# Optimization experiments

Hardware: AMD Instinct MI355X
Metric: run time of the kernel (lower is better)

## Reference

```python
import jax, jax.numpy as jnp
import numpy as np

B, D, H = 1024, 64, 128


def setup_inputs() -> dict:
    key = jax.random.key(0)
    ks = jax.random.split(key, 12)
    s1 = 1.0 / np.sqrt(4 * D)
    sh = 1.0 / np.sqrt(H)
    sd = 1.0 / np.sqrt(D)
    return {
        "x": jax.random.normal(ks[0], (B, D), dtype=jnp.float32),
        # edge_fn: Linear(4D,H) -> ReLU -> Linear(H,H)
        "W1": jax.random.uniform(ks[1], (4 * D, H), minval=-s1, maxval=s1, dtype=jnp.float32),
        "b1": jax.random.uniform(ks[2], (H,), minval=-s1, maxval=s1, dtype=jnp.float32),
        "W2": jax.random.uniform(ks[3], (H, H), minval=-sh, maxval=sh, dtype=jnp.float32),
        "b2": jax.random.uniform(ks[4], (H,), minval=-sh, maxval=sh, dtype=jnp.float32),
        # tau_proj: Linear(D,1) -> Softplus
        "Wt": jax.random.uniform(ks[5], (D, 1), minval=-sd, maxval=sd, dtype=jnp.float32),
        "bt": jax.random.uniform(ks[6], (1,), minval=-sd, maxval=sd, dtype=jnp.float32),
        # agg: Linear(H,H) -> ReLU
        "Wa": jax.random.uniform(ks[7], (H, H), minval=-sh, maxval=sh, dtype=jnp.float32),
        "ba": jax.random.uniform(ks[8], (H,), minval=-sh, maxval=sh, dtype=jnp.float32),
        # res_proj: Linear(D,H)
        "Wr": jax.random.uniform(ks[9], (D, H), minval=-sd, maxval=sd, dtype=jnp.float32),
        "br": jax.random.uniform(ks[10], (H,), minval=-sd, maxval=sd, dtype=jnp.float32),
        # LayerNorm(H)
        "gamma": jnp.ones((H,), dtype=jnp.float32),
        "beta": jnp.zeros((H,), dtype=jnp.float32),
    }


def reference(x, W1, b1, W2, b2, Wt, bt, Wa, ba, Wr, br, gamma, beta):
    d = x.shape[1]
    # Decompose first linear over concat([x_i, x_j, delta, |delta|]) into 4 sub-matmuls;
    # only the |delta| term needs the pairwise [B,B,D] tensor.
    Wi, Wj, Wd, Wab = W1[:d], W1[d:2 * d], W1[2 * d:3 * d], W1[3 * d:]
    ti = x @ Wi            # [B,H] (i-dependent)
    tj = x @ Wj            # [B,H] (j-dependent)
    td = x @ Wd            # [B,H] (delta = x_i - x_j contribution)
    delta = x[:, None, :] - x[None, :, :]             # [B,B,D]
    ta = jnp.einsum('ijd,dh->ijh', jnp.abs(delta), Wab)  # [B,B,H]
    pre = ti[:, None, :] + tj[None, :, :] + td[:, None, :] - td[None, :, :] + ta + b1
    d_proj = jax.nn.relu(pre) @ W2 + b2               # [B,B,H]
    tau = jnp.maximum(jax.nn.softplus(x @ Wt + bt), 0.01) + 1.0  # [B,1]
    h_mean = d_proj.mean(axis=1) / tau                # mean over j
    h = jax.nn.relu(h_mean @ Wa + ba)
    y = h + (x @ Wr + br)
    mu = y.mean(axis=-1, keepdims=True)
    var = ((y - mu) ** 2).mean(axis=-1, keepdims=True)  # biased, like torch LayerNorm
    return (y - mu) * jax.lax.rsqrt(var + 1e-5) * gamma + beta
```

## Files before the change

kernel.cpp:

```cpp
#include <hip/hip_runtime.h>
#include <hip/hip_bf16.h>
#include <math.h>

#define BB 1024
#define DD 64
#define HH 128

typedef _Float16 half8 __attribute__((ext_vector_type(8)));
typedef __fp16 fp16x2 __attribute__((ext_vector_type(2)));
typedef float floatx4 __attribute__((ext_vector_type(4)));

union H8 { fp16x2 p[4]; half8 v; };

__device__ __forceinline__ void async_cp16(const float* g, float* lds_wave_base) {
    __builtin_amdgcn_global_load_lds(
        (const __attribute__((address_space(1))) unsigned int*)g,
        (__attribute__((address_space(3))) unsigned int*)lds_wave_base,
        16, 0, 0);
}

__global__ __launch_bounds__(256) void prep_kernel(
    const float* __restrict__ x, const float* __restrict__ W1,
    const float* __restrict__ b1,
    float* __restrict__ c1, float* __restrict__ c2P,
    _Float16* __restrict__ wpack)
{
    __shared__ float xs[8][DD];
    const int t = threadIdx.x;
    const int i0 = blockIdx.x * 8;
    xs[t >> 6][t & 63] = x[i0 * DD + t];
    xs[4 + (t >> 6)][t & 63] = x[i0 * DD + 256 + t];
    __syncthreads();

    const int ii = t >> 5;
    const int h4 = t & 31;
    const int h = h4 * 4;
    const int i = i0 + ii;

    float4 a1 = {0.f, 0.f, 0.f, 0.f};
    float4 a2 = {0.f, 0.f, 0.f, 0.f};
    #pragma unroll 4
    for (int k = 0; k < DD; k++) {
        float4 wi = *(const float4*)(W1 + k * HH + h);
        float4 wj = *(const float4*)(W1 + (DD + k) * HH + h);
        float4 wd = *(const float4*)(W1 + (2 * DD + k) * HH + h);
        float xv = xs[ii][k];
        a1.x = fmaf(xv, wi.x + wd.x, a1.x);
        a1.y = fmaf(xv, wi.y + wd.y, a1.y);
        a1.z = fmaf(xv, wi.z + wd.z, a1.z);
        a1.w = fmaf(xv, wi.w + wd.w, a1.w);
        a2.x = fmaf(xv, wj.x - wd.x, a2.x);
        a2.y = fmaf(xv, wj.y - wd.y, a2.y);
        a2.z = fmaf(xv, wj.z - wd.z, a2.z);
        a2.w = fmaf(xv, wj.w - wd.w, a2.w);
    }
    float4 b1v = *(const float4*)(b1 + h);
    float4 c1v = {a1.x + b1v.x, a1.y + b1v.y, a1.z + b1v.z, a1.w + b1v.w};
    *(float4*)(c1 + i * HH + h) = c1v;

    const int jl = i & 15;
    float* cb = c2P + (i >> 4) * 2048 + (h >> 6) * 1024 + ((h >> 4) & 3) * 256 + (jl & 3);
    const int p0 = (jl >> 2) * 16 + (h & 15);
    cb[(p0 + 0) * 4] = a2.x;
    cb[(p0 + 1) * 4] = a2.y;
    cb[(p0 + 2) * 4] = a2.z;
    cb[(p0 + 3) * 4] = a2.w;

    if (blockIdx.x < 32) {
        int f = blockIdx.x * 256 + t;
        int jj = f & 7;
        int l  = (f >> 3) & 63;
        int u  = f >> 9;
        int s  = u & 1, t4 = (u >> 1) & 3, hh = u >> 3;
        int k  = s * 32 + ((l >> 4) << 3) + jj;
        int hcol = hh * 64 + t4 * 16 + (l & 15);
        wpack[f] = (_Float16)W1[(3 * DD + k) * HH + hcol];
    }
}

__global__ __launch_bounds__(256, 4) void pair_kernel(
    const float* __restrict__ x, const float* __restrict__ c1,
    const float* __restrict__ c2P, const _Float16* __restrict__ wpack,
    float* __restrict__ Sp)
{
    __shared__ __align__(16) float xs[2][1024];
    __shared__ __align__(16) float c2s[2][1024];

    const int t = threadIdx.x;
    const int wave = t >> 6;
    const int l = t & 63;
    const int quad = l >> 4, lm = l & 15;
    const int bid = blockIdx.x;
    const int ig = bid >> 3;
    const int hh = (bid >> 2) & 1;
    const int jq = bid & 3;
    const int i = ig * 4 + wave;
    const int j0base = jq * 256;
    const int sw = lm & 7;

    async_cp16(x + (j0base + (t >> 4)) * DD + (((t & 15) ^ ((t >> 4) & 7)) << 2),
               &xs[0][0] + wave * 256);
    async_cp16(c2P + (j0base >> 4) * 2048 + hh * 1024 + t * 4,
               &c2s[0][0] + wave * 256);

    float xi[16];
    {
        const float* xg = x + i * DD + quad * 8;
        *(float4*)(xi)      = *(const float4*)(xg);
        *(float4*)(xi + 4)  = *(const float4*)(xg + 4);
        *(float4*)(xi + 8)  = *(const float4*)(xg + 32);
        *(float4*)(xi + 12) = *(const float4*)(xg + 36);
    }
    float c1r[4];
    #pragma unroll
    for (int t4 = 0; t4 < 4; t4++)
        c1r[t4] = c1[i * HH + hh * 64 + t4 * 16 + lm];
    half8 wf[8];
    #pragma unroll
    for (int u = 0; u < 8; u++)
        wf[u] = *(const half8*)(wpack + ((hh * 8 + u) * 64 + l) * 8);

    float S[4] = {0.f, 0.f, 0.f, 0.f};

    for (int tile = 0; tile < 16; ++tile) {
        const int cur = tile & 1;
        __syncthreads();

        if (tile < 15) {
            const int jn = j0base + (tile + 1) * 16;
            async_cp16(x + (jn + (t >> 4)) * DD + (((t & 15) ^ ((t >> 4) & 7)) << 2),
                       &xs[cur ^ 1][0] + wave * 256);
            async_cp16(c2P + (jn >> 4) * 2048 + hh * 1024 + t * 4,
                       &c2s[cur ^ 1][0] + wave * 256);
        }

        floatx4 acc[4];
        #pragma unroll
        for (int t4 = 0; t4 < 4; t4++) {
            float4 c2v = *(const float4*)(&c2s[cur][t4 * 256 + l * 4]);
            acc[t4][0] = c2v.x + c1r[t4];
            acc[t4][1] = c2v.y + c1r[t4];
            acc[t4][2] = c2v.z + c1r[t4];
            acc[t4][3] = c2v.w + c1r[t4];
        }

        const float* xb = &xs[cur][lm * 64];
        float4 a0 = *(const float4*)(xb + (((quad * 2)     ^ sw) << 2));
        float4 a1 = *(const float4*)(xb + (((quad * 2 + 1) ^ sw) << 2));
        float4 a2 = *(const float4*)(xb + (((quad * 2 + 8) ^ sw) << 2));
        float4 a3 = *(const float4*)(xb + (((quad * 2 + 9) ^ sw) << 2));
        H8 af0, af1;
        af0.p[0] = __builtin_amdgcn_cvt_pkrtz(fabsf(xi[0] - a0.x),  fabsf(xi[1] - a0.y));
        af0.p[1] = __builtin_amdgcn_cvt_pkrtz(fabsf(xi[2] - a0.z),  fabsf(xi[3] - a0.w));
        af0.p[2] = __builtin_amdgcn_cvt_pkrtz(fabsf(xi[4] - a1.x),  fabsf(xi[5] - a1.y));
        af0.p[3] = __builtin_amdgcn_cvt_pkrtz(fabsf(xi[6] - a1.z),  fabsf(xi[7] - a1.w));
        af1.p[0] = __builtin_amdgcn_cvt_pkrtz(fabsf(xi[8] - a2.x),  fabsf(xi[9] - a2.y));
        af1.p[1] = __builtin_amdgcn_cvt_pkrtz(fabsf(xi[10] - a2.z), fabsf(xi[11] - a2.w));
        af1.p[2] = __builtin_amdgcn_cvt_pkrtz(fabsf(xi[12] - a3.x), fabsf(xi[13] - a3.y));
        af1.p[3] = __builtin_amdgcn_cvt_pkrtz(fabsf(xi[14] - a3.z), fabsf(xi[15] - a3.w));

        #pragma unroll
        for (int t4 = 0; t4 < 4; t4++) {
            acc[t4] = __builtin_amdgcn_mfma_f32_16x16x32_f16(af0.v, wf[t4 * 2 + 0], acc[t4], 0, 0, 0);
            acc[t4] = __builtin_amdgcn_mfma_f32_16x16x32_f16(af1.v, wf[t4 * 2 + 1], acc[t4], 0, 0, 0);
        }
        #pragma unroll
        for (int t4 = 0; t4 < 4; t4++) {
            S[t4] += fmaxf(acc[t4][0], 0.f);
            S[t4] += fmaxf(acc[t4][1], 0.f);
            S[t4] += fmaxf(acc[t4][2], 0.f);
            S[t4] += fmaxf(acc[t4][3], 0.f);
        }
    }

    #pragma unroll
    for (int t4 = 0; t4 < 4; t4++) {
        S[t4] += __shfl_xor(S[t4], 16, 64);
        S[t4] += __shfl_xor(S[t4], 32, 64);
    }
    if (quad == 0) {
        #pragma unroll
        for (int t4 = 0; t4 < 4; t4++)
            Sp[(jq * BB + i) * HH + hh * 64 + t4 * 16 + lm] = S[t4];
    }
}

__global__ __launch_bounds__(256) void finish_kernel(
    const float* __restrict__ Sp, const float* __restrict__ W2,
    const float* __restrict__ b2, const float* __restrict__ x,
    const float* __restrict__ Wt, const float* __restrict__ bt,
    const float* __restrict__ Wa, const float* __restrict__ ba,
    const float* __restrict__ Wr, const float* __restrict__ br,
    const float* __restrict__ gamma, const float* __restrict__ beta,
    float* __restrict__ out)
{
    __shared__ float Srow[8][HH];
    __shared__ float mrow[8][HH];
    __shared__ float xrowS[8][DD];
    __shared__ float taus[8];
    const int t = threadIdx.x;
    const int ii = t >> 5;
    const int h4 = t & 31;
    const int h = h4 * 4;
    const int i0 = blockIdx.x * 8;
    const int i = i0 + ii;

    {
        float4 s = {0.f, 0.f, 0.f, 0.f};
        #pragma unroll
        for (int q = 0; q < 4; q++) {
            float4 v = *(const float4*)(Sp + (q * BB + i) * HH + h);
            s.x += v.x; s.y += v.y; s.z += v.z; s.w += v.w;
        }
        const float inv = 1.0f / (float)BB;
        float4 sm = {s.x * inv, s.y * inv, s.z * inv, s.w * inv};
        *(float4*)(&Srow[ii][h]) = sm;
    }
    xrowS[t >> 6][t & 63] = x[i0 * DD + t];
    xrowS[4 + (t >> 6)][t & 63] = x[i0 * DD + 256 + t];

    {
        float p = x[i * DD + h4] * Wt[h4] + x[i * DD + 32 + h4] * Wt[32 + h4];
        #pragma unroll
        for (int off = 16; off; off >>= 1) p += __shfl_xor(p, off, 64);
        if (h4 == 0) {
            float z = p + bt[0];
            float sp = (z > 20.f) ? z : log1pf(expf(z));
            taus[ii] = fmaxf(sp, 0.01f) + 1.0f;
        }
    }
    __syncthreads();

    float4 acc = *(const float4*)(b2 + h);
    #pragma unroll 8
    for (int k = 0; k < HH; k++) {
        float4 w = *(const float4*)(W2 + k * HH + h);
        float sv = Srow[ii][k];
        acc.x = fmaf(sv, w.x, acc.x); acc.y = fmaf(sv, w.y, acc.y);
        acc.z = fmaf(sv, w.z, acc.z); acc.w = fmaf(sv, w.w, acc.w);
    }
    const float itau = 1.0f / taus[ii];
    float4 mv = {acc.x * itau, acc.y * itau, acc.z * itau, acc.w * itau};
    *(float4*)(&mrow[ii][h]) = mv;
    __syncthreads();

    float4 a2 = *(const float4*)(ba + h);
    #pragma unroll 8
    for (int k = 0; k < HH; k++) {
        float4 w = *(const float4*)(Wa + k * HH + h);
        float sv = mrow[ii][k];
        a2.x = fmaf(sv, w.x, a2.x); a2.y = fmaf(sv, w.y, a2.y);
        a2.z = fmaf(sv, w.z, a2.z); a2.w = fmaf(sv, w.w, a2.w);
    }
    float4 brv = *(const float4*)(br + h);
    float4 y = {fmaxf(a2.x, 0.f) + brv.x, fmaxf(a2.y, 0.f) + brv.y,
                fmaxf(a2.z, 0.f) + brv.z, fmaxf(a2.w, 0.f) + brv.w};
    #pragma unroll 8
    for (int d = 0; d < DD; d++) {
        float4 w = *(const float4*)(Wr + d * HH + h);
        float xv = xrowS[ii][d];
        y.x = fmaf(xv, w.x, y.x); y.y = fmaf(xv, w.y, y.y);
        y.z = fmaf(xv, w.z, y.z); y.w = fmaf(xv, w.w, y.w);
    }

    float p = y.x + y.y + y.z + y.w;
    #pragma unroll
    for (int off = 16; off; off >>= 1) p += __shfl_xor(p, off, 64);
    float mu = p * (1.0f / (float)HH);
    float4 dy = {y.x - mu, y.y - mu, y.z - mu, y.w - mu};
    float q = dy.x * dy.x + dy.y * dy.y + dy.z * dy.z + dy.w * dy.w;
    #pragma unroll
    for (int off = 16; off; off >>= 1) q += __shfl_xor(q, off, 64);
    float rs = rsqrtf(q * (1.0f / (float)HH) + 1e-5f);
    float4 gv = *(const float4*)(gamma + h);
    float4 bv = *(const float4*)(beta + h);
    float4 o = {dy.x * rs * gv.x + bv.x, dy.y * rs * gv.y + bv.y,
                dy.z * rs * gv.z + bv.z, dy.w * rs * gv.w + bv.w};
    *(float4*)(out + i * HH + h) = o;
}

extern "C" void kernel_launch(void* const* d_in, const int* in_sizes, int n_in,
                              void* d_out, int out_size, void* d_ws, size_t ws_size,
                              hipStream_t stream)
{
    const float* x     = (const float*)d_in[0];
    const float* W1    = (const float*)d_in[1];
    const float* b1    = (const float*)d_in[2];
    const float* W2    = (const float*)d_in[3];
    const float* b2    = (const float*)d_in[4];
    const float* Wt    = (const float*)d_in[5];
    const float* bt    = (const float*)d_in[6];
    const float* Wa    = (const float*)d_in[7];
    const float* ba    = (const float*)d_in[8];
    const float* Wr    = (const float*)d_in[9];
    const float* br    = (const float*)d_in[10];
    const float* gamma = (const float*)d_in[11];
    const float* beta  = (const float*)d_in[12];
    float* out = (float*)d_out;

    char* ws = (char*)d_ws;
    float*     c1    = (float*)(ws);
    float*     c2P   = (float*)(ws + (512 << 10));
    _Float16*  wpack = (_Float16*)(ws + (1024 << 10));
    float*     Sp    = (float*)(ws + (1056 << 10));

    prep_kernel<<<128, 256, 0, stream>>>(x, W1, b1, c1, c2P, wpack);
    pair_kernel<<<2048, 256, 0, stream>>>(x, c1, c2P, wpack, Sp);
    finish_kernel<<<128, 256, 0, stream>>>(Sp, W2, b2, x, Wt, bt,
                                           Wa, ba, Wr, br, gamma, beta, out);
}
```

Baseline: 134.0 us.

## Drop LDS staging in pair kernel; each wave handles two rows with register prefetch

The pair kernel no longer stages j-tiles of x and c2 through double-buffered LDS with async global-to-LDS copies and barriers. Each wave now reads its j-tile directly from global memory into registers, software-pipelined two tiles ahead. Each wave also processes two i rows, so every loaded tile feeds twice the MFMA work. The grid is halved and the occupancy hint is lowered to 2, trading higher register use and fewer resident waves for no block-level synchronisation and less load traffic per unit of work.

```diff
diff --git a/kernel.cpp b/kernel.cpp
--- a/kernel.cpp
+++ b/kernel.cpp
@@ -11,13 +11,6 @@
 typedef float floatx4 __attribute__((ext_vector_type(4)));
 
 union H8 { fp16x2 p[4]; half8 v; };
-
-__device__ __forceinline__ void async_cp16(const float* g, float* lds_wave_base) {
-    __builtin_amdgcn_global_load_lds(
-        (const __attribute__((address_space(1))) unsigned int*)g,
-        (__attribute__((address_space(3))) unsigned int*)lds_wave_base,
-        16, 0, 0);
-}
 
 __global__ __launch_bounds__(256) void prep_kernel(
     const float* __restrict__ x, const float* __restrict__ W1,
@@ -78,111 +71,130 @@
     }
 }
 
-__global__ __launch_bounds__(256, 4) void pair_kernel(
+__device__ __forceinline__ void compute_i(
+    const float4 a0, const float4 a1, const float4 a2, const float4 a3,
+    const float4 c0, const float4 c1q, const float4 c2q, const float4 c3q,
+    const float* xi, const float* c1r, const half8* wf, float* S)
+{
+    floatx4 acc[4];
+    acc[0][0] = c0.x + c1r[0];  acc[0][1] = c0.y + c1r[0];
+    acc[0][2] = c0.z + c1r[0];  acc[0][3] = c0.w + c1r[0];
+    acc[1][0] = c1q.x + c1r[1]; acc[1][1] = c1q.y + c1r[1];
+    acc[1][2] = c1q.z + c1r[1]; acc[1][3] = c1q.w + c1r[1];
+    acc[2][0] = c2q.x + c1r[2]; acc[2][1] = c2q.y + c1r[2];
+    acc[2][2] = c2q.z + c1r[2]; acc[2][3] = c2q.w + c1r[2];
+    acc[3][0] = c3q.x + c1r[3]; acc[3][1] = c3q.y + c1r[3];
+    acc[3][2] = c3q.z + c1r[3]; acc[3][3] = c3q.w + c1r[3];
+
+    H8 af0, af1;
+    af0.p[0] = __builtin_amdgcn_cvt_pkrtz(fabsf(xi[0] - a0.x),  fabsf(xi[1] - a0.y));
+    af0.p[1] = __builtin_amdgcn_cvt_pkrtz(fabsf(xi[2] - a0.z),  fabsf(xi[3] - a0.w));
+    af0.p[2] = __builtin_amdgcn_cvt_pkrtz(fabsf(xi[4] - a1.x),  fabsf(xi[5] - a1.y));
+    af0.p[3] = __builtin_amdgcn_cvt_pkrtz(fabsf(xi[6] - a1.z),  fabsf(xi[7] - a1.w));
+    af1.p[0] = __builtin_amdgcn_cvt_pkrtz(fabsf(xi[8] - a2.x),  fabsf(xi[9] - a2.y));
+    af1.p[1] = __builtin_amdgcn_cvt_pkrtz(fabsf(xi[10] - a2.z), fabsf(xi[11] - a2.w));
+    af1.p[2] = __builtin_amdgcn_cvt_pkrtz(fabsf(xi[12] - a3.x), fabsf(xi[13] - a3.y));
+    af1.p[3] = __builtin_amdgcn_cvt_pkrtz(fabsf(xi[14] - a3.z), fabsf(xi[15] - a3.w));
+
+    #pragma unroll
+    for (int t4 = 0; t4 < 4; t4++) {
+        acc[t4] = __builtin_amdgcn_mfma_f32_16x16x32_f16(af0.v, wf[t4 * 2 + 0], acc[t4], 0, 0, 0);
+        acc[t4] = __builtin_amdgcn_mfma_f32_16x16x32_f16(af1.v, wf[t4 * 2 + 1], acc[t4], 0, 0, 0);
+    }
+    #pragma unroll
+    for (int t4 = 0; t4 < 4; t4++) {
+        S[t4] += fmaxf(acc[t4][0], 0.f);
+        S[t4] += fmaxf(acc[t4][1], 0.f);
+        S[t4] += fmaxf(acc[t4][2], 0.f);
+        S[t4] += fmaxf(acc[t4][3], 0.f);
+    }
+}
+
+__global__ __launch_bounds__(256, 2) void pair_kernel(
     const float* __restrict__ x, const float* __restrict__ c1,
     const float* __restrict__ c2P, const _Float16* __restrict__ wpack,
     float* __restrict__ Sp)
 {
-    __shared__ __align__(16) float xs[2][1024];
-    __shared__ __align__(16) float c2s[2][1024];
-
     const int t = threadIdx.x;
-    const int wave = t >> 6;
+    const int wv = t >> 6;
     const int l = t & 63;
     const int quad = l >> 4, lm = l & 15;
-    const int bid = blockIdx.x;
-    const int ig = bid >> 3;
-    const int hh = (bid >> 2) & 1;
-    const int jq = bid & 3;
-    const int i = ig * 4 + wave;
+    const int w = blockIdx.x * 4 + wv;
+    const int jq = w >> 10;
+    const int hh = (w >> 9) & 1;
+    const int ig2 = w & 511;
+    const int iA = ig2 * 2, iB = iA + 1;
     const int j0base = jq * 256;
-    const int sw = lm & 7;
-
-    async_cp16(x + (j0base + (t >> 4)) * DD + (((t & 15) ^ ((t >> 4) & 7)) << 2),
-               &xs[0][0] + wave * 256);
-    async_cp16(c2P + (j0base >> 4) * 2048 + hh * 1024 + t * 4,
-               &c2s[0][0] + wave * 256);
-
-    float xi[16];
+
+    const float* xrow  = x + (j0base + lm) * DD + quad * 8;
+    const float* cbase = c2P + (jq * 16) * 2048 + hh * 1024 + l * 4;
+
+    float xiA[16], xiB[16];
     {
-        const float* xg = x + i * DD + quad * 8;
-        *(float4*)(xi)      = *(const float4*)(xg);
-        *(float4*)(xi + 4)  = *(const float4*)(xg + 4);
-        *(float4*)(xi + 8)  = *(const float4*)(xg + 32);
-        *(float4*)(xi + 12) = *(const float4*)(xg + 36);
-    }
-    float c1r[4];
-    #pragma unroll
-    for (int t4 = 0; t4 < 4; t4++)
-        c1r[t4] = c1[i * HH + hh * 64 + t4 * 16 + lm];
+        const float* xg = x + iA * DD + quad * 8;
+        *(float4*)(xiA)      = *(const float4*)(xg);
+        *(float4*)(xiA + 4)  = *(const float4*)(xg + 4);
+        *(float4*)(xiA + 8)  = *(const float4*)(xg + 32);
+        *(float4*)(xiA + 12) = *(const float4*)(xg + 36);
+        const float* xh = x + iB * DD + quad * 8;
+        *(float4*)(xiB)      = *(const float4*)(xh);
+        *(float4*)(xiB + 4)  = *(const float4*)(xh + 4);
+        *(float4*)(xiB + 8)  = *(const float4*)(xh + 32);
+        *(float4*)(xiB + 12) = *(const float4*)(xh + 36);
+    }
+    float c1A[4], c1B[4];
+    #pragma unroll
+    for (int t4 = 0; t4 < 4; t4++) {
+        c1A[t4] = c1[iA * HH + hh * 64 + t4 * 16 + lm];
+        c1B[t4] = c1[iB * HH + hh * 64 + t4 * 16 + lm];
+    }
     half8 wf[8];
     #pragma unroll
     for (int u = 0; u < 8; u++)
         wf[u] = *(const half8*)(wpack + ((hh * 8 + u) * 64 + l) * 8);
 
-    float S[4] = {0.f, 0.f, 0.f, 0.f};
-
-    for (int tile = 0; tile < 16; ++tile) {
-        const int cur = tile & 1;
-        __syncthreads();
-
-        if (tile < 15) {
-            const int jn = j0base + (tile + 1) * 16;
-            async_cp16(x + (jn + (t >> 4)) * DD + (((t & 15) ^ ((t >> 4) & 7)) << 2),
-                       &xs[cur ^ 1][0] + wave * 256);
-            async_cp16(c2P + (jn >> 4) * 2048 + hh * 1024 + t * 4,
-                       &c2s[cur ^ 1][0] + wave * 256);
-        }
-
-        floatx4 acc[4];
-        #pragma unroll
-        for (int t4 = 0; t4 < 4; t4++) {
-            float4 c2v = *(const float4*)(&c2s[cur][t4 * 256 + l * 4]);
-            acc[t4][0] = c2v.x + c1r[t4];
-            acc[t4][1] = c2v.y + c1r[t4];
-            acc[t4][2] = c2v.z + c1r[t4];
-            acc[t4][3] = c2v.w + c1r[t4];
-        }
-
-        const float* xb = &xs[cur][lm * 64];
-        float4 a0 = *(const float4*)(xb + (((quad * 2)     ^ sw) << 2));
-        float4 a1 = *(const float4*)(xb + (((quad * 2 + 1) ^ sw) << 2));
-        float4 a2 = *(const float4*)(xb + (((quad * 2 + 8) ^ sw) << 2));
-        float4 a3 = *(const float4*)(xb + (((quad * 2 + 9) ^ sw) << 2));
-        H8 af0, af1;
-        af0.p[0] = __builtin_amdgcn_cvt_pkrtz(fabsf(xi[0] - a0.x),  fabsf(xi[1] - a0.y));
-        af0.p[1] = __builtin_amdgcn_cvt_pkrtz(fabsf(xi[2] - a0.z),  fabsf(xi[3] - a0.w));
-        af0.p[2] = __builtin_amdgcn_cvt_pkrtz(fabsf(xi[4] - a1.x),  fabsf(xi[5] - a1.y));
-        af0.p[3] = __builtin_amdgcn_cvt_pkrtz(fabsf(xi[6] - a1.z),  fabsf(xi[7] - a1.w));
-        af1.p[0] = __builtin_amdgcn_cvt_pkrtz(fabsf(xi[8] - a2.x),  fabsf(xi[9] - a2.y));
-        af1.p[1] = __builtin_amdgcn_cvt_pkrtz(fabsf(xi[10] - a2.z), fabsf(xi[11] - a2.w));
-        af1.p[2] = __builtin_amdgcn_cvt_pkrtz(fabsf(xi[12] - a3.x), fabsf(xi[13] - a3.y));
-        af1.p[3] = __builtin_amdgcn_cvt_pkrtz(fabsf(xi[14] - a3.z), fabsf(xi[15] - a3.w));
-
-        #pragma unroll
-        for (int t4 = 0; t4 < 4; t4++) {
-            acc[t4] = __builtin_amdgcn_mfma_f32_16x16x32_f16(af0.v, wf[t4 * 2 + 0], acc[t4], 0, 0, 0);
-            acc[t4] = __builtin_amdgcn_mfma_f32_16x16x32_f16(af1.v, wf[t4 * 2 + 1], acc[t4], 0, 0, 0);
-        }
-        #pragma unroll
-        for (int t4 = 0; t4 < 4; t4++) {
-            S[t4] += fmaxf(acc[t4][0], 0.f);
-            S[t4] += fmaxf(acc[t4][1], 0.f);
-            S[t4] += fmaxf(acc[t4][2], 0.f);
-            S[t4] += fmaxf(acc[t4][3], 0.f);
-        }
-    }
+    float SA[4] = {0.f, 0.f, 0.f, 0.f};
+    float SB[4] = {0.f, 0.f, 0.f, 0.f};
+
+    float4 A0, A1, A2, A3, C0, C1v, C2v, C3v;
+    float4 B0, B1, B2, B3, D0, D1v, D2v, D3v;
+
+#define LOADT(tt, a0, a1, a2, a3, c0, c1q, c2q, c3q) do {  \
+    const float* xp_ = xrow + ((tt) << 10);                \
+    a0 = *(const float4*)(xp_);                            \
+    a1 = *(const float4*)(xp_ + 4);                        \
+    a2 = *(const float4*)(xp_ + 32);                       \
+    a3 = *(const float4*)(xp_ + 36);                       \
+    const float* cp_ = cbase + ((tt) << 11);               \
+    c0  = *(const float4*)(cp_);                           \
+    c1q = *(const float4*)(cp_ + 256);                     \
+    c2q = *(const float4*)(cp_ + 512);                     \
+    c3q = *(const float4*)(cp_ + 768);                     \
+} while (0)
+
+    LOADT(0, A0, A1, A2, A3, C0, C1v, C2v, C3v);
+    for (int tt = 0; tt < 16; tt += 2) {
+        LOADT(tt + 1, B0, B1, B2, B3, D0, D1v, D2v, D3v);
+        compute_i(A0, A1, A2, A3, C0, C1v, C2v, C3v, xiA, c1A, wf, SA);
+        compute_i(A0, A1, A2, A3, C0, C1v, C2v, C3v, xiB, c1B, wf, SB);
+        if (tt + 2 < 16)
+            LOADT(tt + 2, A0, A1, A2, A3, C0, C1v, C2v, C3v);
+        compute_i(B0, B1, B2, B3, D0, D1v, D2v, D3v, xiA, c1A, wf, SA);
+        compute_i(B0, B1, B2, B3, D0, D1v, D2v, D3v, xiB, c1B, wf, SB);
+    }
+#undef LOADT
 
     #pragma unroll
     for (int t4 = 0; t4 < 4; t4++) {
-        S[t4] += __shfl_xor(S[t4], 16, 64);
-        S[t4] += __shfl_xor(S[t4], 32, 64);
-    }
-    if (quad == 0) {
-        #pragma unroll
-        for (int t4 = 0; t4 < 4; t4++)
-            Sp[(jq * BB + i) * HH + hh * 64 + t4 * 16 + lm] = S[t4];
-    }
+        SA[t4] += __shfl_xor(SA[t4], 16, 64);
+        SA[t4] += __shfl_xor(SA[t4], 32, 64);
+        SB[t4] += __shfl_xor(SB[t4], 16, 64);
+        SB[t4] += __shfl_xor(SB[t4], 32, 64);
+    }
+    float sa = (quad == 0) ? SA[0] : (quad == 1) ? SA[1] : (quad == 2) ? SA[2] : SA[3];
+    float sb = (quad == 0) ? SB[0] : (quad == 1) ? SB[1] : (quad == 2) ? SB[2] : SB[3];
+    Sp[(jq * BB + iA) * HH + hh * 64 + l] = sa;
+    Sp[(jq * BB + iB) * HH + hh * 64 + l] = sb;
 }
 
 __global__ __launch_bounds__(256) void finish_kernel(
@@ -305,7 +317,7 @@
     float*     Sp    = (float*)(ws + (1056 << 10));
 
     prep_kernel<<<128, 256, 0, stream>>>(x, W1, b1, c1, c2P, wpack);
-    pair_kernel<<<2048, 256, 0, stream>>>(x, c1, c2P, wpack, Sp);
+    pair_kernel<<<1024, 256, 0, stream>>>(x, c1, c2P, wpack, Sp);
     finish_kernel<<<128, 256, 0, stream>>>(Sp, W2, b2, x, Wt, bt,
                                            Wa, ba, Wr, br, gamma, beta, out);
 }
```

New measurement: 143.6 us. 7.2% more time.
